# Kernel optimization log

Hardware: AMD Instinct MI355X
Metric: run time of the kernel (lower is better)

## Reference

```python
import jax, jax.numpy as jnp
import numpy as np

N, F, H, R, E = 50000, 128, 128, 8, 800000
BN_EPS = 1e-5


def setup_inputs() -> dict:
    key = jax.random.key(0)
    ks = jax.random.split(key, 10)
    g = lambda k, shp: jax.random.normal(k, shp, dtype=jnp.float32) * (1.0 / np.sqrt(shp[-2] if len(shp) > 1 else shp[-1]))
    return {
        "x": jax.random.normal(ks[0], (N, F), dtype=jnp.float32),
        "edge_index": jax.random.randint(ks[1], (2, E), 0, N, dtype=jnp.int32),
        "edge_type": jax.random.randint(ks[2], (E,), 0, R, dtype=jnp.int32),
        "W1": g(ks[3], (F, H)),
        "b1": jnp.zeros((H,), jnp.float32),
        "weight": g(ks[4], (R, H, H)),
        "root": g(ks[5], (H, H)),
        "bias_c": jnp.zeros((H,), jnp.float32),
        "gamma": jnp.ones((H,), jnp.float32),
        "beta": jnp.zeros((H,), jnp.float32),
        "W2": g(ks[6], (H, H)),
        "b2": jnp.zeros((H,), jnp.float32),
        "Wo": g(ks[7], (H, 1)),
        "bo": jnp.zeros((1,), jnp.float32),
    }


def reference(x, edge_index, edge_type, W1, b1, weight, root, bias_c, gamma, beta, W2, b2, Wo, bo):
    n = x.shape[0]
    r = weight.shape[0]
    src, dst = edge_index[0], edge_index[1]
    # segment id combining relation and destination node: equivalent to the
    # per-relation edge-mask + scatter-add loop in RGCNConv, but in one pass.
    seg = edge_type.astype(jnp.int32) * n + dst

    def conv(h):
        msg = h[src]                                            # [E, H] gather
        agg = jax.ops.segment_sum(msg, seg, num_segments=r * n)  # [R*N, H]
        agg = agg.reshape(r, n, -1)                             # [R, N, H]
        out = jnp.einsum('rnc,rco->no', agg, weight)            # per-relation matmul, summed
        return out + h @ root + bias_c

    def bn(h):
        mu = h.mean(axis=0)
        var = h.var(axis=0)  # biased var, matches torch BN training normalization
        return gamma * (h - mu) * jax.lax.rsqrt(var + BN_EPS) + beta

    h = x @ W1 + b1
    h = jax.nn.relu(bn(conv(h)))
    h = jax.nn.relu(bn(conv(h)))
    h = h @ W2 + b2
    h = h @ Wo + bo
    return jax.nn.sigmoid(h)
```

## Files before the change

### kernel.cpp

```cpp
#include <hip/hip_runtime.h>
#include <stdint.h>

typedef __bf16 bf16;
typedef __bf16 bf16x8 __attribute__((ext_vector_type(8)));
typedef float f32x4 __attribute__((ext_vector_type(4)));

__device__ __forceinline__ float bfbits2f(uint32_t lo16) {
    uint32_t b = lo16 << 16;
    float f;
    __builtin_memcpy(&f, &b, 4);
    return f;
}

__device__ __forceinline__ uint32_t pack2bf(float a, float b) {
    uint32_t lo = __builtin_bit_cast(unsigned short, (bf16)a);
    uint32_t hi = __builtin_bit_cast(unsigned short, (bf16)b);
    return lo | (hi << 16);
}

__device__ __forceinline__ void gload_lds16(const void* g, void* l) {
    __builtin_amdgcn_global_load_lds((const __attribute__((address_space(1))) void*)g,
                                     (__attribute__((address_space(3))) void*)l, 16, 0, 0);
}

__global__ void k_prep(const float* __restrict__ W1, const float* __restrict__ weight,
                       const float* __restrict__ root, const float* __restrict__ W2,
                       const float* __restrict__ b2, const float* __restrict__ Wo,
                       const float* __restrict__ bo, bf16* __restrict__ W1T,
                       bf16* __restrict__ WcatT2, float* __restrict__ qc, int R, int ldt) {
    int total = 16384 * (R + 2);
    for (int i = blockIdx.x * blockDim.x + threadIdx.x; i < total + 129; i += gridDim.x * blockDim.x) {
        if (i < 16384) {
            int f = i >> 7, h = i & 127;
            W1T[h * 128 + f] = (bf16)W1[f * 128 + h];
        } else if (i < total) {
            int j = i - 16384;
            int r = j >> 14, rem = j & 16383, c = rem >> 7, o = rem & 127;
            float v = (r < R) ? weight[(size_t)(r * 128 + c) * 128 + o] : root[c * 128 + o];
            WcatT2[(size_t)o * ldt + r * 128 + c] = (bf16)v;
        } else {
            int t = i - total;
            if (t < 128) {
                float s = 0.f;
                for (int j = 0; j < 128; j++) s += W2[t * 128 + j] * Wo[j];
                qc[t] = s;
            } else {
                float c = bo[0];
                for (int j = 0; j < 128; j++) c += b2[j] * Wo[j];
                qc[128] = c;
            }
        }
    }
}

__global__ void k_hist(const int* __restrict__ dst, const int* __restrict__ etype,
                       int* __restrict__ cnt, int E, int R) {
    for (int e = blockIdx.x * blockDim.x + threadIdx.x; e < E; e += gridDim.x * blockDim.x)
        atomicAdd(&cnt[dst[e] * R + etype[e]], 1);
}

__global__ __launch_bounds__(256) void k_scan_blk(const int* __restrict__ cnt, int* __restrict__ bsum, int M) {
    int i = blockIdx.x * 256 + threadIdx.x;
    int v = (i < M) ? cnt[i] : 0;
#pragma unroll
    for (int d = 1; d < 64; d <<= 1) v += __shfl_xor(v, d);
    __shared__ int ws[4];
    if ((threadIdx.x & 63) == 0) ws[threadIdx.x >> 6] = v;
    __syncthreads();
    if (threadIdx.x == 0) bsum[blockIdx.x] = ws[0] + ws[1] + ws[2] + ws[3];
}

__global__ __launch_bounds__(256) void k_scan_top(int* __restrict__ bsum, int nb) {
    __shared__ int s[256];
    __shared__ int carry;
    int t = threadIdx.x;
    if (t == 0) carry = 0;
    __syncthreads();
    for (int base = 0; base < nb; base += 256) {
        int i = base + t;
        int v = (i < nb) ? bsum[i] : 0;
        s[t] = v;
        __syncthreads();
#pragma unroll
        for (int d = 1; d < 256; d <<= 1) {
            int u = (t >= d) ? s[t - d] : 0;
            __syncthreads();
            s[t] += u;
            __syncthreads();
        }
        int excl = carry + s[t] - v;
        int tot = s[255];
        __syncthreads();
        if (i < nb) bsum[i] = excl;
        if (t == 0) carry += tot;
        __syncthreads();
    }
}

__global__ __launch_bounds__(256) void k_scan_apply(const int* __restrict__ cnt, const int* __restrict__ bsum,
                                                    int* __restrict__ row_off, int* __restrict__ cursor, int M) {
    int b = blockIdx.x, t = threadIdx.x;
    int i = b * 256 + t;
    int v = (i < M) ? cnt[i] : 0;
    int lane = t & 63, wid = t >> 6;
    int incl = v;
#pragma unroll
    for (int d = 1; d < 64; d <<= 1) {
        int u = __shfl_up(incl, d);
        if (lane >= d) incl += u;
    }
    __shared__ int ws[4];
    if (lane == 63) ws[wid] = incl;
    __syncthreads();
    int woff = 0;
    for (int wj = 0; wj < 4; wj++)
        if (wj < wid) woff += ws[wj];
    int excl = bsum[b] + woff + incl - v;
    if (i < M) {
        row_off[i] = excl;
        cursor[i] = excl;
        if (i == M - 1) row_off[M] = excl + v;
    }
}

__global__ void k_fill(const int* __restrict__ src, const int* __restrict__ dst,
                       const int* __restrict__ etype, int* __restrict__ cursor,
                       int* __restrict__ csr, int E, int R, int pbase) {
    int p = blockIdx.x & 7;
    int bg = blockIdx.x >> 3;
    int nchunk = gridDim.x >> 3;
    int chunk = (E + nchunk - 1) / nchunk;
    int beg = bg * chunk, end = min(beg + chunk, E);
    int lo = p * pbase, hi = lo + pbase;
    for (int e = beg + (int)threadIdx.x; e < end; e += blockDim.x) {
        int et = etype[e];
        int seg = dst[e] * R + et;
        if (seg >= lo && seg < hi) {
            int pos = atomicAdd(&cursor[seg], 1);
            csr[pos] = (et << 16) | src[e];
        }
    }
}

__global__ __launch_bounds__(256) void k_gemm0(const float* __restrict__ A, const bf16* __restrict__ BT,
                                               const float* __restrict__ bias, bf16* __restrict__ C, int M) {
    __shared__ bf16 sA[128 * 128];
    __shared__ bf16 sB[128 * 128];
    int tid = threadIdx.x;
    int m0 = blockIdx.x * 128;
#pragma unroll
    for (int i = 0; i < 8; i++) {
        int chunk = i * 256 + tid;
        int row = chunk >> 4, c16 = chunk & 15;
        int sw = ((c16 ^ (row & 7)) << 3);
        int gr = m0 + row;
        int4 va = {0, 0, 0, 0};
        if (gr < M) {
            const float* ap = A + (size_t)gr * 128 + (c16 << 3);
            float4 f0 = *reinterpret_cast<const float4*>(ap);
            float4 f1 = *reinterpret_cast<const float4*>(ap + 4);
            bf16 tmp[8] = {(bf16)f0.x, (bf16)f0.y, (bf16)f0.z, (bf16)f0.w,
                           (bf16)f1.x, (bf16)f1.y, (bf16)f1.z, (bf16)f1.w};
            __builtin_memcpy(&va, tmp, 16);
        }
        *reinterpret_cast<int4*>(&sA[row * 128 + sw]) = va;
        int4 vb = *reinterpret_cast<const int4*>(&BT[(size_t)row * 128 + (c16 << 3)]);
        *reinterpret_cast<int4*>(&sB[row * 128 + sw]) = vb;
    }
    __syncthreads();

    int lane = tid & 63, w = tid >> 6;
    int wm = (w >> 1) * 64, wn = (w & 1) * 64;
    int lr = lane & 15, lk = lane >> 4;
    f32x4 zero = {0.f, 0.f, 0.f, 0.f};
    f32x4 acc[4][4];
#pragma unroll
    for (int mi = 0; mi < 4; mi++)
#pragma unroll
        for (int ni = 0; ni < 4; ni++) acc[mi][ni] = zero;

#pragma unroll
    for (int kk = 0; kk < 4; kk++) {
        int c = (kk << 2) + lk;
        bf16x8 af[4], bfr[4];
#pragma unroll
        for (int mi = 0; mi < 4; mi++) {
            int r = wm + mi * 16 + lr;
            af[mi] = *reinterpret_cast<const bf16x8*>(&sA[r * 128 + ((c ^ (r & 7)) << 3)]);
        }
#pragma unroll
        for (int ni = 0; ni < 4; ni++) {
            int r = wn + ni * 16 + lr;
            bfr[ni] = *reinterpret_cast<const bf16x8*>(&sB[r * 128 + ((c ^ (r & 7)) << 3)]);
        }
#pragma unroll
        for (int mi = 0; mi < 4; mi++)
#pragma unroll
            for (int ni = 0; ni < 4; ni++)
                acc[mi][ni] = __builtin_amdgcn_mfma_f32_16x16x32_bf16(af[mi], bfr[ni], acc[mi][ni], 0, 0, 0);
    }

#pragma unroll
    for (int ni = 0; ni < 4; ni++) {
        int col = wn + ni * 16 + lr;
        float bia = bias[col];
#pragma unroll
        for (int mi = 0; mi < 4; mi++) {
#pragma unroll
            for (int j = 0; j < 4; j++) {
                int row = m0 + wm + mi * 16 + lk * 4 + j;
                if (row < M) C[(size_t)row * 128 + col] = (bf16)(acc[mi][ni][j] + bia);
            }
        }
    }
}

__global__ __launch_bounds__(128) void k_agg2(const bf16* __restrict__ h, const int* __restrict__ row_off,
                                              const int* __restrict__ csr, bf16* __restrict__ G, int N, int R) {
    __shared__ float acc[2][8 * 128];
    int wi = threadIdx.x >> 6;
    int n = blockIdx.x * 2 + wi;
    if (n >= N) return;
    int lane = threadIdx.x & 63;
    int c0 = lane * 2;
    float* a = acc[wi];
#pragma unroll
    for (int i = 0; i < 16; i++) a[i * 64 + lane] = 0.f;
    int beg = row_off[n * R], end = row_off[n * R + R];
    int cur = -1;
    float a0 = 0.f, a1 = 0.f;
    int i = beg;
    for (; i + 4 <= end; i += 4) {
        int p0 = csr[i], p1 = csr[i + 1], p2 = csr[i + 2], p3 = csr[i + 3];
        uint32_t v0 = *reinterpret_cast<const uint32_t*>(&h[(size_t)(p0 & 0xffff) * 128 + c0]);
        uint32_t v1 = *reinterpret_cast<const uint32_t*>(&h[(size_t)(p1 & 0xffff) * 128 + c0]);
        uint32_t v2 = *reinterpret_cast<const uint32_t*>(&h[(size_t)(p2 & 0xffff) * 128 + c0]);
        uint32_t v3 = *reinterpret_cast<const uint32_t*>(&h[(size_t)(p3 & 0xffff) * 128 + c0]);
        {
            int r = p0 >> 16; bool s = (r == cur);
            a0 = (s ? a0 : 0.f) + bfbits2f(v0 & 0xffffu);
            a1 = (s ? a1 : 0.f) + bfbits2f(v0 >> 16);
            cur = r;
            float2 st = {a0, a1};
            *reinterpret_cast<float2*>(&a[r * 128 + c0]) = st;
        }
        {
            int r = p1 >> 16; bool s = (r == cur);
            a0 = (s ? a0 : 0.f) + bfbits2f(v1 & 0xffffu);
            a1 = (s ? a1 : 0.f) + bfbits2f(v1 >> 16);
            cur = r;
            float2 st = {a0, a1};
            *reinterpret_cast<float2*>(&a[r * 128 + c0]) = st;
        }
        {
            int r = p2 >> 16; bool s = (r == cur);
            a0 = (s ? a0 : 0.f) + bfbits2f(v2 & 0xffffu);
            a1 = (s ? a1 : 0.f) + bfbits2f(v2 >> 16);
            cur = r;
            float2 st = {a0, a1};
            *reinterpret_cast<float2*>(&a[r * 128 + c0]) = st;
        }
        {
            int r = p3 >> 16; bool s = (r == cur);
            a0 = (s ? a0 : 0.f) + bfbits2f(v3 & 0xffffu);
            a1 = (s ? a1 : 0.f) + bfbits2f(v3 >> 16);
            cur = r;
            float2 st = {a0, a1};
            *reinterpret_cast<float2*>(&a[r * 128 + c0]) = st;
        }
    }
    for (; i < end; i++) {
        int p = csr[i];
        uint32_t v = *reinterpret_cast<const uint32_t*>(&h[(size_t)(p & 0xffff) * 128 + c0]);
        int r = p >> 16; bool s = (r == cur);
        a0 = (s ? a0 : 0.f) + bfbits2f(v & 0xffffu);
        a1 = (s ? a1 : 0.f) + bfbits2f(v >> 16);
        cur = r;
        float2 st = {a0, a1};
        *reinterpret_cast<float2*>(&a[r * 128 + c0]) = st;
    }
    size_t gbase = (size_t)n * 1024 + c0;
#pragma unroll
    for (int r = 0; r < 8; r++) {
        __builtin_nontemporal_store(pack2bf(a[r * 128 + c0], a[r * 128 + c0 + 1]),
                                    reinterpret_cast<uint32_t*>(&G[gbase + r * 128]));
    }
}

__global__ __launch_bounds__(256) void k_gemm2(const bf16* __restrict__ G, const bf16* __restrict__ hsrc,
                                               const bf16* __restrict__ BT, const float* __restrict__ bias,
                                               float* __restrict__ C, float* __restrict__ stats,
                                               int M, int K) {
    __shared__ bf16 sA[128 * 128];
    __shared__ float csum[128], csum2[128];
    int tid = threadIdx.x;
    if (tid < 128) { csum[tid] = 0.f; csum2[tid] = 0.f; }
    int m0 = blockIdx.x * 128;
    int lane = tid & 63, w = tid >> 6;
    int wm = (w >> 1) * 64, wn = (w & 1) * 64;
    int lr = lane & 15, lk = lane >> 4;
    int l4 = lane >> 4, c16 = lane & 15;
    f32x4 zero = {0.f, 0.f, 0.f, 0.f};
    f32x4 acc[4][4];
#pragma unroll
    for (int mi = 0; mi < 4; mi++)
#pragma unroll
        for (int ni = 0; ni < 4; ni++) acc[mi][ni] = zero;

    int KT = K >> 7;
    size_t ldg = (size_t)(K - 128);
    for (int kt = 0; kt < KT; kt++) {
        bool lastt = (kt == KT - 1);
        const bf16* Abase = lastt ? hsrc : G;
        size_t ldA = lastt ? 128 : ldg;
        int ka = lastt ? 0 : (kt << 7);
        int k0 = kt << 7;
#pragma unroll
        for (int i = 0; i < 8; i++) {
            int row = i * 16 + (w << 2) + l4;
            int cs = (c16 ^ (row & 7)) << 3;
            int gr = m0 + row;
            gr = gr < M ? gr : M - 1;
            gload_lds16(Abase + (size_t)gr * ldA + ka + cs, &sA[(i * 256 + (w << 6)) * 8]);
        }
        asm volatile("s_waitcnt vmcnt(0)" ::: "memory");
        __syncthreads();

#pragma unroll
        for (int kk = 0; kk < 4; kk++) {
            int c = (kk << 2) + lk;
            bf16x8 af[4], bfr[4];
#pragma unroll
            for (int mi = 0; mi < 4; mi++) {
                int r = wm + mi * 16 + lr;
                af[mi] = *reinterpret_cast<const bf16x8*>(&sA[r * 128 + ((c ^ (r & 7)) << 3)]);
            }
#pragma unroll
            for (int ni = 0; ni < 4; ni++) {
                int o = wn + ni * 16 + lr;
                bfr[ni] = *reinterpret_cast<const bf16x8*>(&BT[(size_t)o * K + k0 + (c << 3)]);
            }
#pragma unroll
            for (int mi = 0; mi < 4; mi++)
#pragma unroll
                for (int ni = 0; ni < 4; ni++)
                    acc[mi][ni] = __builtin_amdgcn_mfma_f32_16x16x32_bf16(af[mi], bfr[ni], acc[mi][ni], 0, 0, 0);
        }
        __syncthreads();
    }

    float ls[4], ls2[4];
#pragma unroll
    for (int ni = 0; ni < 4; ni++) { ls[ni] = 0.f; ls2[ni] = 0.f; }
#pragma unroll
    for (int ni = 0; ni < 4; ni++) {
        int col = wn + ni * 16 + lr;
        float bia = bias[col];
#pragma unroll
        for (int mi = 0; mi < 4; mi++) {
#pragma unroll
            for (int j = 0; j < 4; j++) {
                int row = m0 + wm + mi * 16 + lk * 4 + j;
                if (row < M) {
                    float val = acc[mi][ni][j] + bia;
                    C[(size_t)row * 128 + col] = val;
                    ls[ni] += val;
                    ls2[ni] += val * val;
                }
            }
        }
    }
#pragma unroll
    for (int ni = 0; ni < 4; ni++) {
        float s = ls[ni], s2 = ls2[ni];
        s += __shfl_xor(s, 16); s += __shfl_xor(s, 32);
        s2 += __shfl_xor(s2, 16); s2 += __shfl_xor(s2, 32);
        if (lk == 0) {
            int col = wn + ni * 16 + lr;
            atomicAdd(&csum[col], s);
            atomicAdd(&csum2[col], s2);
        }
    }
    __syncthreads();
    if (tid < 128) {
        atomicAdd(&stats[tid], csum[tid]);
        atomicAdd(&stats[128 + tid], csum2[tid]);
    }
}

__global__ void k_bnrelu(const float* __restrict__ conv, const float* __restrict__ stats,
                         const float* __restrict__ gamma, const float* __restrict__ beta,
                         bf16* __restrict__ h, int N, float invN) {
    int total = N * 32;
    for (int i = blockIdx.x * blockDim.x + threadIdx.x; i < total; i += gridDim.x * blockDim.x) {
        int c4 = (i & 31) << 2;
        float4 v = *reinterpret_cast<const float4*>(&conv[(size_t)i * 4]);
        const float* vv = &v.x;
        uint64_t pk = 0;
#pragma unroll
        for (int j = 0; j < 4; j++) {
            int c = c4 + j;
            float mu = stats[c] * invN;
            float var = stats[128 + c] * invN - mu * mu;
            float sc = gamma[c] * rsqrtf(var + 1e-5f);
            float sh = beta[c] - mu * sc;
            float val = fmaxf(vv[j] * sc + sh, 0.f);
            unsigned short us = __builtin_bit_cast(unsigned short, (bf16)val);
            pk |= (uint64_t)us << (16 * j);
        }
        *reinterpret_cast<uint64_t*>(&h[(size_t)i * 4]) = pk;
    }
}

__global__ __launch_bounds__(256) void k_bnout(const float* __restrict__ conv, const float* __restrict__ stats,
                                               const float* __restrict__ gamma, const float* __restrict__ beta,
                                               const float* __restrict__ qc, float* __restrict__ out,
                                               int N, float invN) {
    int wi = threadIdx.x >> 6;
    int n = blockIdx.x * 4 + wi;
    if (n >= N) return;
    int lane = threadIdx.x & 63;
    int c0 = lane * 2;
    float mu0 = stats[c0] * invN;
    float var0 = stats[128 + c0] * invN - mu0 * mu0;
    float sc0 = gamma[c0] * rsqrtf(var0 + 1e-5f);
    float sh0 = beta[c0] - mu0 * sc0;
    float mu1 = stats[c0 + 1] * invN;
    float var1 = stats[128 + c0 + 1] * invN - mu1 * mu1;
    float sc1 = gamma[c0 + 1] * rsqrtf(var1 + 1e-5f);
    float sh1 = beta[c0 + 1] - mu1 * sc1;
    float2 v = *reinterpret_cast<const float2*>(&conv[(size_t)n * 128 + c0]);
    float v0 = fmaxf(v.x * sc0 + sh0, 0.f);
    float v1 = fmaxf(v.y * sc1 + sh1, 0.f);
    float s = v0 * qc[c0] + v1 * qc[c0 + 1];
#pragma unroll
    for (int d = 1; d < 64; d <<= 1) s += __shfl_xor(s, d);
    if (lane == 0) out[n] = 1.f / (1.f + expf(-(s + qc[128])));
}

extern "C" void kernel_launch(void* const* d_in, const int* in_sizes, int n_in,
                              void* d_out, int out_size, void* d_ws, size_t ws_size,
                              hipStream_t stream) {
    const float* x      = (const float*)d_in[0];
    const int*   ei     = (const int*)d_in[1];
    const int*   etype  = (const int*)d_in[2];
    const float* W1     = (const float*)d_in[3];
    const float* b1     = (const float*)d_in[4];
    const float* weight = (const float*)d_in[5];
    const float* root   = (const float*)d_in[6];
    const float* bias_c = (const float*)d_in[7];
    const float* gamma  = (const float*)d_in[8];
    const float* beta   = (const float*)d_in[9];
    const float* W2     = (const float*)d_in[10];
    const float* b2     = (const float*)d_in[11];
    const float* Wo     = (const float*)d_in[12];
    const float* bo     = (const float*)d_in[13];
    float* out = (float*)d_out;

    int H = in_sizes[4];
    int F = in_sizes[3] / H;
    int N = in_sizes[0] / F;
    int E = in_sizes[2];
    int R = in_sizes[5] / (H * H);
    int ldt = (R + 1) * H;
    int M = N * R;

    const int* srcv = ei;
    const int* dstv = ei + E;

    char* p = (char*)d_ws;
    auto alloc = [&](size_t bytes) -> char* {
        char* r = p;
        p += (bytes + 255) & ~(size_t)255;
        return r;
    };
    bf16*  G       = (bf16*)alloc((size_t)N * (R * H) * 2);
    bf16*  h       = (bf16*)alloc((size_t)N * H * 2);
    float* conv    = (float*)alloc((size_t)N * H * 4);
    bf16*  WcatT2  = (bf16*)alloc((size_t)ldt * H * 2);
    bf16*  W1T     = (bf16*)alloc((size_t)F * H * 2);
    float* qc      = (float*)alloc(129 * 4);
    int*   cnt     = (int*)alloc((size_t)M * 4);
    int*   row_off = (int*)alloc((size_t)(M + 1) * 4);
    int*   cursor  = (int*)alloc((size_t)M * 4);
    int*   csr     = (int*)alloc((size_t)E * 4);
    float* stats   = (float*)alloc(512 * 4);
    int*   bsum    = (int*)alloc(2048 * 4);
    if ((size_t)(p - (char*)d_ws) > ws_size) return;

    int nb = (M + 255) / 256;
    int pbase = (M + 7) / 8;

    hipMemsetAsync(cnt, 0, (size_t)M * 4, stream);
    hipMemsetAsync(stats, 0, 512 * 4, stream);
    k_prep<<<256, 256, 0, stream>>>(W1, weight, root, W2, b2, Wo, bo, W1T, WcatT2, qc, R, ldt);
    k_hist<<<1024, 256, 0, stream>>>(dstv, etype, cnt, E, R);
    k_scan_blk<<<nb, 256, 0, stream>>>(cnt, bsum, M);
    k_scan_top<<<1, 256, 0, stream>>>(bsum, nb);
    k_scan_apply<<<nb, 256, 0, stream>>>(cnt, bsum, row_off, cursor, M);
    k_fill<<<1024, 256, 0, stream>>>(srcv, dstv, etype, cursor, csr, E, R, pbase);

    int mb = (N + 127) / 128;
    k_gemm0<<<mb, 256, 0, stream>>>(x, W1T, b1, h, N);

    float invN = 1.f / (float)N;
    for (int l = 0; l < 2; l++) {
        float* statsl = stats + l * 256;
        k_agg2<<<(N + 1) / 2, 128, 0, stream>>>(h, row_off, csr, G, N, R);
        k_gemm2<<<mb, 256, 0, stream>>>(G, h, WcatT2, bias_c, conv, statsl, N, ldt);
        if (l == 0)
            k_bnrelu<<<2048, 256, 0, stream>>>(conv, statsl, gamma, beta, h, N, invN);
        else
            k_bnout<<<(N + 3) / 4, 256, 0, stream>>>(conv, statsl, gamma, beta, qc, out, N, invN);
    }
}
```

Measured before the change: 343.3 us.

## Precompute edge seg/payload, widen agg gather unroll, stage gemm2 B tile in LDS

Three changes. The histogram kernel now writes each edge's segment id and packed payload, so the partitioned fill pass reads two arrays instead of re-reading src, dst and etype on each of its 8 partition sweeps. The aggregation kernel issues 8 independent gathers per iteration instead of 4, giving more memory-level parallelism. The main GEMM stages the weight tile into swizzled LDS with async global-to-LDS loads rather than reading B fragments straight from global memory. The cost is 32 KB more LDS per GEMM block, which lowers occupancy, plus two extra E-sized workspace arrays.

```diff
diff --git a/kernel.cpp b/kernel.cpp
--- a/kernel.cpp
+++ b/kernel.cpp
@@ -53,10 +53,16 @@
     }
 }
 
-__global__ void k_hist(const int* __restrict__ dst, const int* __restrict__ etype,
-                       int* __restrict__ cnt, int E, int R) {
-    for (int e = blockIdx.x * blockDim.x + threadIdx.x; e < E; e += gridDim.x * blockDim.x)
-        atomicAdd(&cnt[dst[e] * R + etype[e]], 1);
+__global__ void k_hist(const int* __restrict__ src, const int* __restrict__ dst,
+                       const int* __restrict__ etype, int* __restrict__ cnt,
+                       int* __restrict__ seg, int* __restrict__ pay, int E, int R) {
+    for (int e = blockIdx.x * blockDim.x + threadIdx.x; e < E; e += gridDim.x * blockDim.x) {
+        int et = etype[e];
+        int s = dst[e] * R + et;
+        seg[e] = s;
+        pay[e] = (et << 16) | src[e];
+        atomicAdd(&cnt[s], 1);
+    }
 }
 
 __global__ __launch_bounds__(256) void k_scan_blk(const int* __restrict__ cnt, int* __restrict__ bsum, int M) {
@@ -123,9 +129,8 @@
     }
 }
 
-__global__ void k_fill(const int* __restrict__ src, const int* __restrict__ dst,
-                       const int* __restrict__ etype, int* __restrict__ cursor,
-                       int* __restrict__ csr, int E, int R, int pbase) {
+__global__ void k_fill(const int* __restrict__ seg, const int* __restrict__ pay,
+                       int* __restrict__ cursor, int* __restrict__ csr, int E, int pbase) {
     int p = blockIdx.x & 7;
     int bg = blockIdx.x >> 3;
     int nchunk = gridDim.x >> 3;
@@ -133,11 +138,10 @@
     int beg = bg * chunk, end = min(beg + chunk, E);
     int lo = p * pbase, hi = lo + pbase;
     for (int e = beg + (int)threadIdx.x; e < end; e += blockDim.x) {
-        int et = etype[e];
-        int seg = dst[e] * R + et;
-        if (seg >= lo && seg < hi) {
-            int pos = atomicAdd(&cursor[seg], 1);
-            csr[pos] = (et << 16) | src[e];
+        int s = seg[e];
+        if (s >= lo && s < hi) {
+            int pos = atomicAdd(&cursor[s], 1);
+            csr[pos] = pay[e];
         }
     }
 }
@@ -230,49 +234,30 @@
     int cur = -1;
     float a0 = 0.f, a1 = 0.f;
     int i = beg;
-    for (; i + 4 <= end; i += 4) {
-        int p0 = csr[i], p1 = csr[i + 1], p2 = csr[i + 2], p3 = csr[i + 3];
-        uint32_t v0 = *reinterpret_cast<const uint32_t*>(&h[(size_t)(p0 & 0xffff) * 128 + c0]);
-        uint32_t v1 = *reinterpret_cast<const uint32_t*>(&h[(size_t)(p1 & 0xffff) * 128 + c0]);
-        uint32_t v2 = *reinterpret_cast<const uint32_t*>(&h[(size_t)(p2 & 0xffff) * 128 + c0]);
-        uint32_t v3 = *reinterpret_cast<const uint32_t*>(&h[(size_t)(p3 & 0xffff) * 128 + c0]);
-        {
-            int r = p0 >> 16; bool s = (r == cur);
-            a0 = (s ? a0 : 0.f) + bfbits2f(v0 & 0xffffu);
-            a1 = (s ? a1 : 0.f) + bfbits2f(v0 >> 16);
+    for (; i + 8 <= end; i += 8) {
+        int pp[8];
+        uint32_t vv[8];
+#pragma unroll
+        for (int u = 0; u < 8; u++) pp[u] = csr[i + u];
+#pragma unroll
+        for (int u = 0; u < 8; u++)
+            vv[u] = *reinterpret_cast<const uint32_t*>(&h[(size_t)(pp[u] & 0xffff) * 128 + c0]);
+#pragma unroll
+        for (int u = 0; u < 8; u++) {
+            int r = pp[u] >> 16;
+            bool s = (r == cur);
+            a0 = (s ? a0 : 0.f) + bfbits2f(vv[u] & 0xffffu);
+            a1 = (s ? a1 : 0.f) + bfbits2f(vv[u] >> 16);
             cur = r;
             float2 st = {a0, a1};
             *reinterpret_cast<float2*>(&a[r * 128 + c0]) = st;
         }
-        {
-            int r = p1 >> 16; bool s = (r == cur);
-            a0 = (s ? a0 : 0.f) + bfbits2f(v1 & 0xffffu);
-            a1 = (s ? a1 : 0.f) + bfbits2f(v1 >> 16);
-            cur = r;
-            float2 st = {a0, a1};
-            *reinterpret_cast<float2*>(&a[r * 128 + c0]) = st;
-        }
-        {
-            int r = p2 >> 16; bool s = (r == cur);
-            a0 = (s ? a0 : 0.f) + bfbits2f(v2 & 0xffffu);
-            a1 = (s ? a1 : 0.f) + bfbits2f(v2 >> 16);
-            cur = r;
-            float2 st = {a0, a1};
-            *reinterpret_cast<float2*>(&a[r * 128 + c0]) = st;
-        }
-        {
-            int r = p3 >> 16; bool s = (r == cur);
-            a0 = (s ? a0 : 0.f) + bfbits2f(v3 & 0xffffu);
-            a1 = (s ? a1 : 0.f) + bfbits2f(v3 >> 16);
-            cur = r;
-            float2 st = {a0, a1};
-            *reinterpret_cast<float2*>(&a[r * 128 + c0]) = st;
-        }
     }
     for (; i < end; i++) {
         int p = csr[i];
         uint32_t v = *reinterpret_cast<const uint32_t*>(&h[(size_t)(p & 0xffff) * 128 + c0]);
-        int r = p >> 16; bool s = (r == cur);
+        int r = p >> 16;
+        bool s = (r == cur);
         a0 = (s ? a0 : 0.f) + bfbits2f(v & 0xffffu);
         a1 = (s ? a1 : 0.f) + bfbits2f(v >> 16);
         cur = r;
@@ -292,6 +277,7 @@
                                                float* __restrict__ C, float* __restrict__ stats,
                                                int M, int K) {
     __shared__ bf16 sA[128 * 128];
+    __shared__ bf16 sB[128 * 128];
     __shared__ float csum[128], csum2[128];
     int tid = threadIdx.x;
     if (tid < 128) { csum[tid] = 0.f; csum2[tid] = 0.f; }
@@ -322,6 +308,7 @@
             int gr = m0 + row;
             gr = gr < M ? gr : M - 1;
             gload_lds16(Abase + (size_t)gr * ldA + ka + cs, &sA[(i * 256 + (w << 6)) * 8]);
+            gload_lds16(&BT[(size_t)row * K + k0 + cs], &sB[(i * 256 + (w << 6)) * 8]);
         }
         asm volatile("s_waitcnt vmcnt(0)" ::: "memory");
         __syncthreads();
@@ -337,8 +324,8 @@
             }
 #pragma unroll
             for (int ni = 0; ni < 4; ni++) {
-                int o = wn + ni * 16 + lr;
-                bfr[ni] = *reinterpret_cast<const bf16x8*>(&BT[(size_t)o * K + k0 + (c << 3)]);
+                int r = wn + ni * 16 + lr;
+                bfr[ni] = *reinterpret_cast<const bf16x8*>(&sB[r * 128 + ((c ^ (r & 7)) << 3)]);
             }
 #pragma unroll
             for (int mi = 0; mi < 4; mi++)
@@ -484,6 +471,8 @@
     int*   row_off = (int*)alloc((size_t)(M + 1) * 4);
     int*   cursor  = (int*)alloc((size_t)M * 4);
     int*   csr     = (int*)alloc((size_t)E * 4);
+    int*   seg     = (int*)alloc((size_t)E * 4);
+    int*   pay     = (int*)alloc((size_t)E * 4);
     float* stats   = (float*)alloc(512 * 4);
     int*   bsum    = (int*)alloc(2048 * 4);
     if ((size_t)(p - (char*)d_ws) > ws_size) return;
@@ -494,11 +483,11 @@
     hipMemsetAsync(cnt, 0, (size_t)M * 4, stream);
     hipMemsetAsync(stats, 0, 512 * 4, stream);
     k_prep<<<256, 256, 0, stream>>>(W1, weight, root, W2, b2, Wo, bo, W1T, WcatT2, qc, R, ldt);
-    k_hist<<<1024, 256, 0, stream>>>(dstv, etype, cnt, E, R);
+    k_hist<<<1024, 256, 0, stream>>>(srcv, dstv, etype, cnt, seg, pay, E, R);
     k_scan_blk<<<nb, 256, 0, stream>>>(cnt, bsum, M);
     k_scan_top<<<1, 256, 0, stream>>>(bsum, nb);
     k_scan_apply<<<nb, 256, 0, stream>>>(cnt, bsum, row_off, cursor, M);
-    k_fill<<<1024, 256, 0, stream>>>(srcv, dstv, etype, cursor, csr, E, R, pbase);
+    k_fill<<<1024, 256, 0, stream>>>(seg, pay, cursor, csr, E, pbase);
 
     int mb = (N + 127) / 128;
     k_gemm0<<<mb, 256, 0, stream>>>(x, W1T, b1, h, N);
```

After: 305.7 us. -11.0%, faster.
